# Optimization experiments

Hardware: AMD Instinct MI355X
Metric: run time of the kernel (lower is better)

Reference implementation:

```python
import jax, jax.numpy as jnp
import numpy as np

B, S, H, D = 2, 2048, 16, 64
HID = H * D
THETA = 10000.0
SCALING_FACTOR = 1
NEG_INF = -1e9


def _rope_cos_sin(position_ids):
    # Llama RoPE: inv_freq over even dims, duplicated halves.
    inv_freq = 1.0 / (THETA ** (jnp.arange(0, D, 2, dtype=jnp.float32) / D))  # [D/2]
    freqs = position_ids.astype(jnp.float32)[..., None] * inv_freq            # [B,S,D/2]
    emb = jnp.concatenate([freqs, freqs], axis=-1)                            # [B,S,D]
    return jnp.cos(emb), jnp.sin(emb)


def _rotate_half(x):
    x1, x2 = jnp.split(x, 2, axis=-1)
    return jnp.concatenate([-x2, x1], axis=-1)


def setup_inputs() -> dict:
    key = jax.random.key(0)
    ks = jax.random.split(key, 6)
    return {
        "hidden_states": jax.random.normal(ks[0], (B, S, HID), dtype=jnp.float32),
        "info_embeddings": jax.random.normal(ks[1], (B, S, HID), dtype=jnp.float32) * 0.1,
        "Wq": jax.random.normal(ks[2], (HID, HID), dtype=jnp.float32) * 0.02,
        "Wk": jax.random.normal(ks[3], (HID, HID), dtype=jnp.float32) * 0.02,
        "Wv": jax.random.normal(ks[4], (HID, HID), dtype=jnp.float32) * 0.02,
        "Wo": jax.random.normal(ks[5], (HID, HID), dtype=jnp.float32) * 0.02,
        "position_ids": jnp.broadcast_to(jnp.arange(S, dtype=jnp.int64), (B, S)),
    }


def reference(hidden_states, info_embeddings, Wq, Wk, Wv, Wo, position_ids):
    b, s, _ = hidden_states.shape
    # projections -> [B,H,S,D]
    q = (hidden_states @ Wq).reshape(b, s, H, D).transpose(0, 2, 1, 3)
    k = (hidden_states @ Wk).reshape(b, s, H, D).transpose(0, 2, 1, 3)
    v = (hidden_states @ Wv).reshape(b, s, H, D).transpose(0, 2, 1, 3)
    # info embedding added to q and k (pre-RoPE)
    info = info_embeddings.reshape(b, s, H, D).transpose(0, 2, 1, 3)
    q = q + info
    k = k + info
    # rotary position embedding
    cos, sin = _rope_cos_sin(position_ids)
    cos = cos[:, None]  # [B,1,S,D]
    sin = sin[:, None]
    q = q * cos + _rotate_half(q) * sin
    k = k * cos + _rotate_half(k) * sin
    # eager attention with custom scaling
    scale = 1.0 / float(np.sqrt(SCALING_FACTOR * D))
    scores = jnp.einsum("bhqd,bhkd->bhqk", q, k) * scale  # [B,H,S,S]
    causal = jnp.tril(jnp.ones((s, s), dtype=bool))
    scores = scores + jnp.where(causal, 0.0, NEG_INF).astype(scores.dtype)
    probs = jax.nn.softmax(scores, axis=-1)  # dropout p=0 (eval)
    attn = jnp.einsum("bhqk,bhkd->bhqd", probs, v)
    attn = attn.transpose(0, 2, 1, 3).reshape(b, s, HID)
    return attn @ Wo
```

## Files before the change

### kernel.cpp

```cpp
#include <hip/hip_runtime.h>
#include <hip/hip_bf16.h>

#define HB 2
#define HS 2048
#define HH 16
#define HD 64
#define HIDN 1024
#define MROWS 4096

typedef __attribute__((ext_vector_type(8))) short s16x8;
typedef __attribute__((ext_vector_type(4))) float f32x4;
typedef unsigned short u16;

__device__ inline u16 f2bf(float f) {
  union { __hip_bfloat16 h; u16 u; } cvt;
  cvt.h = __float2bfloat16(f);
  return cvt.u;
}

__device__ __forceinline__ void gload16(const u16* g, u16* l) {
  __builtin_amdgcn_global_load_lds((const __attribute__((address_space(1))) void*)g,
                                   (__attribute__((address_space(3))) void*)l, 16, 0, 0);
}

__global__ __launch_bounds__(256) void k_prep(const float* __restrict__ hs,
                                              const float* __restrict__ W0, const float* __restrict__ W1,
                                              const float* __restrict__ W2, const float* __restrict__ W3,
                                              u16* __restrict__ Wt, u16* __restrict__ Xbf) {
  const int bid = blockIdx.x;
  if (bid < 1024) {
    const int z = bid >> 8, y = (bid >> 4) & 15, x = bid & 15;
    const float* W = (z == 0) ? W0 : (z == 1) ? W1 : (z == 2) ? W2 : W3;
    u16* O = Wt + (size_t)z * HIDN * HIDN;
    __shared__ float tile[64][65];
    int k0 = y * 64, c0 = x * 64;
    #pragma unroll
    for (int i = 0; i < 16; ++i) {
      int id = threadIdx.x + i * 256;
      int r = id >> 6, c = id & 63;
      tile[r][c] = W[(size_t)(k0 + r) * HIDN + c0 + c];
    }
    __syncthreads();
    #pragma unroll
    for (int i = 0; i < 16; ++i) {
      int id = threadIdx.x + i * 256;
      int r = id >> 6, c = id & 63;
      O[(size_t)(c0 + r) * HIDN + k0 + c] = f2bf(tile[c][r]);
    }
  } else {
    int i = ((bid - 1024) * 256 + threadIdx.x) * 4;
    float4 a = *(const float4*)(hs + i);
    ushort4 r;
    r.x = f2bf(a.x); r.y = f2bf(a.y); r.z = f2bf(a.z); r.w = f2bf(a.w);
    *(ushort4*)(Xbf + i) = r;
  }
}

#define BM 128
#define BN 128
#define BK 64
#define LDK 72

__global__ __launch_bounds__(256) void k_qkv(const u16* __restrict__ X, const u16* __restrict__ Wt,
                                             const float* __restrict__ info,
                                             u16* __restrict__ Qb, u16* __restrict__ Kb, u16* __restrict__ Vt) {
  __shared__ __align__(16) u16 smem[128 * 136];
  const int bid = blockIdx.x;
  const int g   = bid & 7;
  const int idx = bid >> 3;
  const int nt  = idx & 7;
  const int ml  = (idx >> 3) & 3;
  const int z   = idx >> 5;
  const int mt  = g * 4 + ml;
  const u16* Bt = Wt + (size_t)z * HIDN * HIDN;
  const int tid = threadIdx.x;
  const int lane = tid & 63, wave = tid >> 6;
  const int wr = wave >> 1, wc = wave & 1;
  const int lg = lane >> 4, li = lane & 15;
  const int bm0 = mt * BM, bn0 = nt * BN;

  const int srow = lane >> 3;
  const int scol = (lane & 7) * 8;

  f32x4 acc[4][4];
  #pragma unroll
  for (int m = 0; m < 4; ++m)
    #pragma unroll
    for (int n = 0; n < 4; ++n) acc[m][n] = (f32x4){0.f, 0.f, 0.f, 0.f};

  for (int k0 = 0; k0 < HIDN; k0 += BK) {
    __syncthreads();
    #pragma unroll
    for (int c = 0; c < 4; ++c) {
      const int ci = wave * 4 + c;
      const int row = ci * 8 + srow;
      gload16(X  + (size_t)(bm0 + row) * HIDN + k0 + scol, &smem[ci * 512]);
      gload16(Bt + (size_t)(bn0 + row) * HIDN + k0 + scol, &smem[8192 + ci * 512]);
    }
    __syncthreads();
    #pragma unroll
    for (int kk = 0; kk < 2; ++kk) {
      s16x8 af[4], bfr[4];
      #pragma unroll
      for (int m = 0; m < 4; ++m) af[m]  = *(const s16x8*)(&smem[(wr * 64 + m * 16 + li) * 64 + kk * 32 + lg * 8]);
      #pragma unroll
      for (int n = 0; n < 4; ++n) bfr[n] = *(const s16x8*)(&smem[8192 + (wc * 64 + n * 16 + li) * 64 + kk * 32 + lg * 8]);
      __builtin_amdgcn_s_setprio(1);
      #pragma unroll
      for (int m = 0; m < 4; ++m)
        #pragma unroll
        for (int n = 0; n < 4; ++n)
          acc[m][n] = __builtin_amdgcn_mfma_f32_16x16x32_bf16(af[m], bfr[n], acc[m][n], 0, 0, 0);
      __builtin_amdgcn_s_setprio(0);
    }
  }

  if (z < 2) {
    u16* dst = (z == 0) ? Qb : Kb;
    float invr[2];
    #pragma unroll
    for (int n = 0; n < 2; ++n)
      invr[n] = exp2f(-0.41524101186092030f * (float)(n * 16 + li)) * 0.15915494309189535f;
    #pragma unroll
    for (int m = 0; m < 4; ++m) {
      #pragma unroll
      for (int r = 0; r < 4; ++r) {
        int t = bm0 + wr * 64 + m * 16 + lg * 4 + r;
        int b = t >> 11, s = t & (HS - 1);
        #pragma unroll
        for (int n = 0; n < 2; ++n) {
          int c1 = bn0 + wc * 64 + n * 16 + li;
          float v1 = acc[m][n][r]     + info[(size_t)t * HIDN + c1];
          float v2 = acc[m][n + 2][r] + info[(size_t)t * HIDN + c1 + 32];
          float rev = (float)s * invr[n];
          rev -= floorf(rev);
          float sn = __builtin_amdgcn_sinf(rev);
          float cs = __builtin_amdgcn_cosf(rev);
          float o1 = v1 * cs - v2 * sn;
          float o2 = v2 * cs + v1 * sn;
          if (z == 0) { o1 *= 0.18033688011f; o2 *= 0.18033688011f; }
          int h = c1 >> 6, d1 = c1 & 63;
          size_t base = ((size_t)(b * HH + h) * HS + s) * HD;
          dst[base + d1]      = f2bf(o1);
          dst[base + d1 + 32] = f2bf(o2);
        }
      }
    }
  } else {
    __syncthreads();
    #pragma unroll
    for (int m = 0; m < 4; ++m)
      #pragma unroll
      for (int n = 0; n < 4; ++n)
        #pragma unroll
        for (int r = 0; r < 4; ++r) {
          int cl = wc * 64 + n * 16 + li;
          int ml2 = wr * 64 + m * 16 + lg * 4 + r;
          smem[cl * 136 + ml2] = f2bf(acc[m][n][r]);
        }
    __syncthreads();
    const int b = bm0 >> 11, s0 = bm0 & (HS - 1);
    #pragma unroll
    for (int p = 0; p < 8; ++p) {
      int id = tid + p * 256;
      int cl = id >> 4, m8 = (id & 15) * 8;
      int c = bn0 + cl;
      int h = c >> 6, d = c & 63;
      s16x8 v = *(const s16x8*)(&smem[cl * 136 + m8]);
      *(s16x8*)(&Vt[((size_t)(b * HH + h) * HD + d) * HS + s0 + m8]) = v;
    }
  }
}

__global__ __launch_bounds__(256, 3) void k_attn(const u16* __restrict__ Qb, const u16* __restrict__ Kb,
                                                 const u16* __restrict__ Vt, u16* __restrict__ attnOut) {
  __shared__ u16 Ks[2][64 * LDK];
  __shared__ u16 Vs[2][64 * LDK];
  __shared__ u16 Ps[4][16 * LDK];
  const int bidx = blockIdx.x;
  const int bh = bidx & 31;
  const int j  = 31 - (bidx >> 5);
  const int q0 = j * 64;
  const int ntiles = j + 1;

  const u16* Qh = Qb + (size_t)bh * HS * HD;
  const u16* Kh = Kb + (size_t)bh * HS * HD;
  const u16* Vh = Vt + (size_t)bh * HD * HS;
  const int tid = threadIdx.x;
  const int lane = tid & 63, w = tid >> 6;
  const int lg = lane >> 4, li = lane & 15;
  const int b = bh >> 4, h = bh & 15;

  const int row16 = tid >> 3;
  const int col8  = (tid & 7) * 8;

  s16x8 qf[2];
  #pragma unroll
  for (int kk = 0; kk < 2; ++kk)
    qf[kk] = *(const s16x8*)(Qh + (size_t)(q0 + w * 16 + li) * HD + kk * 32 + lg * 8);

  s16x8 vones;
  #pragma unroll
  for (int e = 0; e < 8; ++e) vones[e] = (short)0x3F80;

  f32x4 o[4];
  #pragma unroll
  for (int n = 0; n < 4; ++n) o[n] = (f32x4){0.f, 0.f, 0.f, 0.f};
  f32x4 ol = (f32x4){0.f, 0.f, 0.f, 0.f};

  {
    uint4 ka = *(const uint4*)(Kh + (size_t)row16 * HD + col8);
    uint4 kb = *(const uint4*)(Kh + (size_t)(row16 + 32) * HD + col8);
    uint4 va = *(const uint4*)(Vh + (size_t)row16 * HS + col8);
    uint4 vb = *(const uint4*)(Vh + (size_t)(row16 + 32) * HS + col8);
    *(uint4*)(&Ks[0][row16 * LDK + col8])        = ka;
    *(uint4*)(&Ks[0][(row16 + 32) * LDK + col8]) = kb;
    *(uint4*)(&Vs[0][row16 * LDK + col8])        = va;
    *(uint4*)(&Vs[0][(row16 + 32) * LDK + col8]) = vb;
  }
  __syncthreads();

  for (int t = 0; t < ntiles; ++t) {
    const int cur = t & 1;
    uint4 rKa, rKb, rVa, rVb;
    const bool more = (t + 1 < ntiles);
    if (more) {
      const int kv1 = (t + 1) * 64;
      rKa = *(const uint4*)(Kh + (size_t)(kv1 + row16) * HD + col8);
      rKb = *(const uint4*)(Kh + (size_t)(kv1 + row16 + 32) * HD + col8);
      rVa = *(const uint4*)(Vh + (size_t)row16 * HS + kv1 + col8);
      rVb = *(const uint4*)(Vh + (size_t)(row16 + 32) * HS + kv1 + col8);
    }

    f32x4 sc[4];
    #pragma unroll
    for (int n = 0; n < 4; ++n) sc[n] = (f32x4){0.f, 0.f, 0.f, 0.f};
    __builtin_amdgcn_s_setprio(1);
    #pragma unroll
    for (int kk = 0; kk < 2; ++kk) {
      #pragma unroll
      for (int n = 0; n < 4; ++n) {
        s16x8 kfr = *(const s16x8*)(&Ks[cur][(n * 16 + li) * LDK + kk * 32 + lg * 8]);
        sc[n] = __builtin_amdgcn_mfma_f32_16x16x32_bf16(kfr, qf[kk], sc[n], 0, 0, 0);
      }
    }
    __builtin_amdgcn_s_setprio(0);

    if (t == ntiles - 1) {
      const int qrel = w * 16 + li;
      #pragma unroll
      for (int n = 0; n < 4; ++n)
        #pragma unroll
        for (int r = 0; r < 4; ++r)
          if (n * 16 + lg * 4 + r > qrel) sc[n][r] = -1e9f;
    }

    #pragma unroll
    for (int n = 0; n < 4; ++n) {
      float p0 = exp2f(sc[n][0]);
      float p1 = exp2f(sc[n][1]);
      float p2 = exp2f(sc[n][2]);
      float p3 = exp2f(sc[n][3]);
      unsigned a0 = __float_as_uint(p0) + 0x8000u;
      unsigned a1 = __float_as_uint(p1) + 0x8000u;
      unsigned a2 = __float_as_uint(p2) + 0x8000u;
      unsigned a3 = __float_as_uint(p3) + 0x8000u;
      uint2 wv;
      wv.x = __builtin_amdgcn_perm(a1, a0, 0x07060302u);
      wv.y = __builtin_amdgcn_perm(a3, a2, 0x07060302u);
      *(uint2*)(&Ps[w][li * LDK + n * 16 + lg * 4]) = wv;
    }

    __builtin_amdgcn_s_setprio(1);
    #pragma unroll
    for (int kk = 0; kk < 2; ++kk) {
      s16x8 pf = *(const s16x8*)(&Ps[w][li * LDK + kk * 32 + lg * 8]);
      #pragma unroll
      for (int n = 0; n < 4; ++n) {
        s16x8 vf = *(const s16x8*)(&Vs[cur][(n * 16 + li) * LDK + kk * 32 + lg * 8]);
        o[n] = __builtin_amdgcn_mfma_f32_16x16x32_bf16(pf, vf, o[n], 0, 0, 0);
      }
      ol = __builtin_amdgcn_mfma_f32_16x16x32_bf16(pf, vones, ol, 0, 0, 0);
    }
    __builtin_amdgcn_s_setprio(0);

    if (more) {
      *(uint4*)(&Ks[cur ^ 1][row16 * LDK + col8])        = rKa;
      *(uint4*)(&Ks[cur ^ 1][(row16 + 32) * LDK + col8]) = rKb;
      *(uint4*)(&Vs[cur ^ 1][row16 * LDK + col8])        = rVa;
      *(uint4*)(&Vs[cur ^ 1][(row16 + 32) * LDK + col8]) = rVb;
      __syncthreads();
    }
  }

  float linvq[4];
  #pragma unroll
  for (int r = 0; r < 4; ++r) linvq[r] = 1.0f / ol[r];
  #pragma unroll
  for (int n = 0; n < 4; ++n)
    #pragma unroll
    for (int r = 0; r < 4; ++r) {
      int srow = q0 + w * 16 + lg * 4 + r;
      attnOut[(size_t)(b * HS + srow) * HIDN + h * 64 + n * 16 + li] = f2bf(o[n][r] * linvq[r]);
    }
}

__global__ __launch_bounds__(256) void k_out(const u16* __restrict__ A, const u16* __restrict__ Bt,
                                             float* __restrict__ out) {
  __shared__ __align__(16) u16 As[BM * 64];
  __shared__ __align__(16) u16 Bs[BN * 64];
  const int bid = blockIdx.x;
  const int g   = bid & 7;
  const int idx = bid >> 3;
  const int nt  = idx & 7;
  const int ml  = idx >> 3;
  const int mt  = g * 4 + ml;
  const int tid = threadIdx.x;
  const int lane = tid & 63, wave = tid >> 6;
  const int wr = wave >> 1, wc = wave & 1;
  const int lg = lane >> 4, li = lane & 15;
  const int bm0 = mt * BM, bn0 = nt * BN;

  const int srow = lane >> 3;
  const int scol = (lane & 7) * 8;

  f32x4 acc[4][4];
  #pragma unroll
  for (int m = 0; m < 4; ++m)
    #pragma unroll
    for (int n = 0; n < 4; ++n) acc[m][n] = (f32x4){0.f, 0.f, 0.f, 0.f};

  for (int k0 = 0; k0 < HIDN; k0 += BK) {
    __syncthreads();
    #pragma unroll
    for (int c = 0; c < 4; ++c) {
      const int ci = wave * 4 + c;
      const int row = ci * 8 + srow;
      gload16(A  + (size_t)(bm0 + row) * HIDN + k0 + scol, &As[ci * 512]);
      gload16(Bt + (size_t)(bn0 + row) * HIDN + k0 + scol, &Bs[ci * 512]);
    }
    __syncthreads();
    #pragma unroll
    for (int kk = 0; kk < 2; ++kk) {
      s16x8 af[4], bfr[4];
      #pragma unroll
      for (int m = 0; m < 4; ++m) af[m]  = *(const s16x8*)(&As[(wr * 64 + m * 16 + li) * 64 + kk * 32 + lg * 8]);
      #pragma unroll
      for (int n = 0; n < 4; ++n) bfr[n] = *(const s16x8*)(&Bs[(wc * 64 + n * 16 + li) * 64 + kk * 32 + lg * 8]);
      __builtin_amdgcn_s_setprio(1);
      #pragma unroll
      for (int m = 0; m < 4; ++m)
        #pragma unroll
        for (int n = 0; n < 4; ++n)
          acc[m][n] = __builtin_amdgcn_mfma_f32_16x16x32_bf16(af[m], bfr[n], acc[m][n], 0, 0, 0);
      __builtin_amdgcn_s_setprio(0);
    }
  }

  #pragma unroll
  for (int m = 0; m < 4; ++m)
    #pragma unroll
    for (int r = 0; r < 4; ++r) {
      int t = bm0 + wr * 64 + m * 16 + lg * 4 + r;
      #pragma unroll
      for (int n = 0; n < 4; ++n) {
        int c = bn0 + wc * 64 + n * 16 + li;
        out[(size_t)t * HIDN + c] = acc[m][n][r];
      }
    }
}

extern "C" void kernel_launch(void* const* d_in, const int* in_sizes, int n_in,
                              void* d_out, int out_size, void* d_ws, size_t ws_size,
                              hipStream_t stream) {
  const float* hs   = (const float*)d_in[0];
  const float* info = (const float*)d_in[1];
  const float* Wq   = (const float*)d_in[2];
  const float* Wk   = (const float*)d_in[3];
  const float* Wv   = (const float*)d_in[4];
  const float* Wo   = (const float*)d_in[5];
  float* out = (float*)d_out;

  char* ws = (char*)d_ws;
  u16* Xbf  = (u16*)(ws);
  u16* Wt   = (u16*)(ws + ((size_t)8  << 20));
  u16* Qb   = (u16*)(ws + ((size_t)16 << 20));
  u16* Kb   = (u16*)(ws + ((size_t)24 << 20));
  u16* Vt   = (u16*)(ws + ((size_t)32 << 20));
  u16* attn = Xbf;

  k_prep<<<dim3(1024 + MROWS * HIDN / 1024), 256, 0, stream>>>(hs, Wq, Wk, Wv, Wo, Wt, Xbf);
  k_qkv<<<dim3(768), 256, 0, stream>>>(Xbf, Wt, info, Qb, Kb, Vt);
  k_attn<<<dim3(1024), 256, 0, stream>>>(Qb, Kb, Vt, attn);
  k_out<<<dim3(256), 256, 0, stream>>>(attn, Wt + (size_t)3 * HIDN * HIDN, out);
}
```

Baseline: 112.6 us.

## Pre-pack info embeddings to bf16 pairs and stage Q/K epilogue through LDS

```diff
diff --git a/kernel.cpp b/kernel.cpp
--- a/kernel.cpp
+++ b/kernel.cpp
@@ -26,7 +26,9 @@
 __global__ __launch_bounds__(256) void k_prep(const float* __restrict__ hs,
                                               const float* __restrict__ W0, const float* __restrict__ W1,
                                               const float* __restrict__ W2, const float* __restrict__ W3,
-                                              u16* __restrict__ Wt, u16* __restrict__ Xbf) {
+                                              const float* __restrict__ info,
+                                              u16* __restrict__ Wt, u16* __restrict__ Xbf,
+                                              unsigned* __restrict__ infoP) {
   const int bid = blockIdx.x;
   if (bid < 1024) {
     const int z = bid >> 8, y = (bid >> 4) & 15, x = bid & 15;
@@ -47,12 +49,27 @@
       int r = id >> 6, c = id & 63;
       O[(size_t)(c0 + r) * HIDN + k0 + c] = f2bf(tile[c][r]);
     }
-  } else {
+  } else if (bid < 5120) {
     int i = ((bid - 1024) * 256 + threadIdx.x) * 4;
     float4 a = *(const float4*)(hs + i);
     ushort4 r;
     r.x = f2bf(a.x); r.y = f2bf(a.y); r.z = f2bf(a.z); r.w = f2bf(a.w);
     *(ushort4*)(Xbf + i) = r;
+  } else {
+    int idx = (bid - 5120) * 256 + threadIdx.x;
+    int o4 = idx * 4;
+    int pi  = o4 & 31;
+    int t16h = o4 >> 5;
+    int h = t16h & 15, t = t16h >> 4;
+    const float* src = info + (size_t)t * HIDN + h * 64 + pi;
+    float4 a = *(const float4*)(src);
+    float4 c = *(const float4*)(src + 32);
+    uint4 w;
+    w.x = (unsigned)f2bf(a.x) | ((unsigned)f2bf(c.x) << 16);
+    w.y = (unsigned)f2bf(a.y) | ((unsigned)f2bf(c.y) << 16);
+    w.z = (unsigned)f2bf(a.z) | ((unsigned)f2bf(c.z) << 16);
+    w.w = (unsigned)f2bf(a.w) | ((unsigned)f2bf(c.w) << 16);
+    *(uint4*)(infoP + o4) = w;
   }
 }
 
@@ -62,7 +79,7 @@
 #define LDK 72
 
 __global__ __launch_bounds__(256) void k_qkv(const u16* __restrict__ X, const u16* __restrict__ Wt,
-                                             const float* __restrict__ info,
+                                             const unsigned* __restrict__ infoP,
                                              u16* __restrict__ Qb, u16* __restrict__ Kb, u16* __restrict__ Vt) {
   __shared__ __align__(16) u16 smem[128 * 136];
   const int bid = blockIdx.x;
@@ -115,8 +132,12 @@
     }
   }
 
+  const int b = bm0 >> 11, s0 = bm0 & (HS - 1);
+  __syncthreads();
+
   if (z < 2) {
     u16* dst = (z == 0) ? Qb : Kb;
+    const int hI = (bn0 >> 6) + wc;
     float invr[2];
     #pragma unroll
     for (int n = 0; n < 2; ++n)
@@ -125,13 +146,14 @@
     for (int m = 0; m < 4; ++m) {
       #pragma unroll
       for (int r = 0; r < 4; ++r) {
-        int t = bm0 + wr * 64 + m * 16 + lg * 4 + r;
-        int b = t >> 11, s = t & (HS - 1);
+        int tl = wr * 64 + m * 16 + lg * 4 + r;
+        int t  = bm0 + tl;
+        int s  = t & (HS - 1);
         #pragma unroll
         for (int n = 0; n < 2; ++n) {
-          int c1 = bn0 + wc * 64 + n * 16 + li;
-          float v1 = acc[m][n][r]     + info[(size_t)t * HIDN + c1];
-          float v2 = acc[m][n + 2][r] + info[(size_t)t * HIDN + c1 + 32];
+          unsigned ip = infoP[((size_t)t * HH + hI) * 32 + n * 16 + li];
+          float v1 = acc[m][n][r]     + __uint_as_float(ip << 16);
+          float v2 = acc[m][n + 2][r] + __uint_as_float(ip & 0xffff0000u);
           float rev = (float)s * invr[n];
           rev -= floorf(rev);
           float sn = __builtin_amdgcn_sinf(rev);
@@ -139,15 +161,22 @@
           float o1 = v1 * cs - v2 * sn;
           float o2 = v2 * cs + v1 * sn;
           if (z == 0) { o1 *= 0.18033688011f; o2 *= 0.18033688011f; }
-          int h = c1 >> 6, d1 = c1 & 63;
-          size_t base = ((size_t)(b * HH + h) * HS + s) * HD;
-          dst[base + d1]      = f2bf(o1);
-          dst[base + d1 + 32] = f2bf(o2);
+          int cl = wc * 64 + n * 16 + li;
+          smem[tl * 136 + cl]      = f2bf(o1);
+          smem[tl * 136 + cl + 32] = f2bf(o2);
         }
       }
     }
+    __syncthreads();
+    #pragma unroll
+    for (int p = 0; p < 8; ++p) {
+      int id = tid + p * 256;
+      int row = id >> 4, ch = (id & 15) * 8;
+      int h = (bn0 >> 6) + (ch >> 6), d = ch & 63;
+      s16x8 v = *(const s16x8*)(&smem[row * 136 + ch]);
+      *(s16x8*)(&dst[((size_t)(b * HH + h) * HS + s0 + row) * HD + d]) = v;
+    }
   } else {
-    __syncthreads();
     #pragma unroll
     for (int m = 0; m < 4; ++m)
       #pragma unroll
@@ -159,7 +188,6 @@
           smem[cl * 136 + ml2] = f2bf(acc[m][n][r]);
         }
     __syncthreads();
-    const int b = bm0 >> 11, s0 = bm0 & (HS - 1);
     #pragma unroll
     for (int p = 0; p < 8; ++p) {
       int id = tid + p * 256;
@@ -387,10 +415,11 @@
   u16* Qb   = (u16*)(ws + ((size_t)16 << 20));
   u16* Kb   = (u16*)(ws + ((size_t)24 << 20));
   u16* Vt   = (u16*)(ws + ((size_t)32 << 20));
+  unsigned* infoP = (unsigned*)(ws + ((size_t)40 << 20));
   u16* attn = Xbf;
 
-  k_prep<<<dim3(1024 + MROWS * HIDN / 1024), 256, 0, stream>>>(hs, Wq, Wk, Wv, Wo, Wt, Xbf);
-  k_qkv<<<dim3(768), 256, 0, stream>>>(Xbf, Wt, info, Qb, Kb, Vt);
+  k_prep<<<dim3(1024 + 4096 + 2048), 256, 0, stream>>>(hs, Wq, Wk, Wv, Wo, info, Wt, Xbf, infoP);
+  k_qkv<<<dim3(768), 256, 0, stream>>>(Xbf, Wt, infoP, Qb, Kb, Vt);
   k_attn<<<dim3(1024), 256, 0, stream>>>(Qb, Kb, Vt, attn);
   k_out<<<dim3(256), 256, 0, stream>>>(attn, Wt + (size_t)3 * HIDN * HIDN, out);
 }
```

Result: slower. 115.6 us (+2.7%).
